# Optimization experiments

Hardware: AMD Instinct MI355X
Metric: run time of the kernel (lower is better)

Reference implementation:

```python
import jax, jax.numpy as jnp
import numpy as np

B, S, D, H, Dh = 2, 1024, 2048, 16, 128
EPS = 1e-6


def setup_inputs() -> dict:
    key = jax.random.key(0)
    ks = jax.random.split(key, 8)
    hidden_states = jax.random.normal(ks[0], (B, S, D), jnp.float32)
    def qweight(k):
        return jax.random.randint(k, (D, D), -127, 128, dtype=jnp.int32)
    wq, wk, wv, wo = qweight(ks[1]), qweight(ks[2]), qweight(ks[3]), qweight(ks[4])
    def scale(k):
        # per-output-channel dequant scale ~ O(1/(127*sqrt(D)))
        return jax.random.uniform(k, (D,), jnp.float32, 0.5, 1.5) / (127.0 * np.sqrt(D))
    wq_s, wk_s, wv_s, wo_s = scale(ks[5]), scale(ks[6]), scale(ks[7]), scale(jax.random.fold_in(key, 99))
    qn_w = jnp.ones((D,), jnp.float32)
    kn_w = jnp.ones((D,), jnp.float32)
    # RoPE tables (rotate-half convention): [S, Dh]
    pos = jnp.arange(S, dtype=jnp.float32)
    inv_freq = 1.0 / (10000.0 ** (jnp.arange(0, Dh, 2, dtype=jnp.float32) / Dh))
    freqs = pos[:, None] * inv_freq[None, :]              # [S, Dh/2]
    cos = jnp.concatenate([jnp.cos(freqs)] * 2, axis=-1)  # [S, Dh]
    sin = jnp.concatenate([jnp.sin(freqs)] * 2, axis=-1)
    lengths = jnp.array([S, 3 * S // 4], dtype=jnp.int32)
    return dict(hidden_states=hidden_states, wq_s=wq_s, wk_s=wk_s, wv_s=wv_s,
                wo_s=wo_s, qn_w=qn_w, kn_w=kn_w, cos=cos, sin=sin,
                wq=wq, wk=wk, wv=wv, wo=wo, lengths=lengths)


def _q8_linear(x, w_int, scale):
    # Q8Linear: int8 weight [out,in] dequantized by per-output-channel scale
    w = w_int.astype(jnp.float32) * scale[:, None]
    return jnp.einsum('bsd,od->bso', x, w)


def _rms_norm(x, w):
    var = jnp.mean(jnp.square(x), axis=-1, keepdims=True)
    return x * jax.lax.rsqrt(var + EPS) * w


def _apply_rope(x, cos, sin):
    # x: [B,S,D] -> per-head rotate-half RoPE -> [B,S,D]
    xh = x.reshape(B, S, H, Dh)
    x1, x2 = jnp.split(xh, 2, axis=-1)
    rot = jnp.concatenate([-x2, x1], axis=-1)
    out = xh * cos[None, :, None, :] + rot * sin[None, :, None, :]
    return out.reshape(B, S, D)


def reference(hidden_states, wq_s, wk_s, wv_s, wo_s, qn_w, kn_w, cos, sin,
              wq, wk, wv, wo, lengths):
    q = _rms_norm(_q8_linear(hidden_states, wq, wq_s), qn_w)
    k = _rms_norm(_q8_linear(hidden_states, wk, wk_s), kn_w)
    v = _q8_linear(hidden_states, wv, wv_s)
    q = _apply_rope(q, cos, sin)
    k = _apply_rope(k, cos, sin)
    # [B,S,D] -> [B,H,S,Dh]
    q = q.reshape(B, S, H, Dh).transpose(0, 2, 1, 3)
    k = k.reshape(B, S, H, Dh).transpose(0, 2, 1, 3)
    v = v.reshape(B, S, H, Dh).transpose(0, 2, 1, 3)
    # length mask -> additive bias [B,1,1,S]
    positions = jnp.arange(S)
    valid = positions[None, :] < lengths[:, None]
    bias = jnp.where(valid, 0.0, -jnp.inf).astype(jnp.float32)[:, None, None, :]
    scores = jnp.einsum('bhqd,bhkd->bhqk', q, k) / np.sqrt(Dh) + bias
    probs = jax.nn.softmax(scores, axis=-1)
    attn = jnp.einsum('bhqk,bhkd->bhqd', probs, v)
    attn = attn.transpose(0, 2, 1, 3).reshape(B, S, D)
    out = _q8_linear(attn, wo, wo_s)
    return out
```

## Files before the change

### kernel.cpp

```cpp
#include <hip/hip_runtime.h>
#include <stdint.h>

typedef __bf16 bf16;
typedef bf16 bf16x8 __attribute__((ext_vector_type(8)));
typedef bf16 bf16x4 __attribute__((ext_vector_type(4)));
typedef float f32x4 __attribute__((ext_vector_type(4)));

#define B_   2
#define S_   1024
#define D_   2048
#define H_   16
#define DH_  128
#define M_   (B_*S_)
#define EPSF 1e-6f

__device__ __forceinline__ void gload_lds16(const void* g, void* l) {
    __builtin_amdgcn_global_load_lds(
        (const __attribute__((address_space(1))) void*)g,
        (__attribute__((address_space(3))) void*)l,
        16, 0, 0);
}

struct ConvArgs {
    const void* s[5];
    bf16* d[5];
};

__global__ __launch_bounds__(256) void conv_all(ConvArgs a, int n) {
    const int z = blockIdx.y;
    const int i = (blockIdx.x * 256 + threadIdx.x) * 8;
    if (i + 8 > n) return;
    bf16x8 o;
    if (z == 0) {
        const float* src = (const float*)a.s[0];
        float4 v0 = *(const float4*)(src + i);
        float4 v1 = *(const float4*)(src + i + 4);
        o[0] = (bf16)v0.x; o[1] = (bf16)v0.y; o[2] = (bf16)v0.z; o[3] = (bf16)v0.w;
        o[4] = (bf16)v1.x; o[5] = (bf16)v1.y; o[6] = (bf16)v1.z; o[7] = (bf16)v1.w;
    } else {
        const int* src = (const int*)a.s[z];
        int4 v0 = *(const int4*)(src + i);
        int4 v1 = *(const int4*)(src + i + 4);
        o[0] = (bf16)(float)v0.x; o[1] = (bf16)(float)v0.y;
        o[2] = (bf16)(float)v0.z; o[3] = (bf16)(float)v0.w;
        o[4] = (bf16)(float)v1.x; o[5] = (bf16)(float)v1.y;
        o[6] = (bf16)(float)v1.z; o[7] = (bf16)(float)v1.w;
    }
    *(bf16x8*)(a.d[z] + i) = o;
}

struct QKVArgs {
    const float* Sc[3];
    bf16* qO; bf16* kO; bf16* vO;
};

__global__ __launch_bounds__(512, 2) void gemmQKV(const bf16* __restrict__ A, const bf16* __restrict__ Wcat,
                                                  QKVArgs args) {
    __shared__ char lds[114688];
    constexpr int NT = D_ / 64;
    constexpr int BUF = 57344;
    const int t = threadIdx.x;
    const int w = t >> 6, l = t & 63;
    const int wr = w >> 2, wc = w & 3;
    const int m0 = blockIdx.y * 256, n0 = blockIdx.x * 192;
    const int hi = l >> 4, lo = l & 15;

    const int r8 = l >> 3;
    const int ce = ((l & 7) ^ (r8 & 7)) * 8;
    const bf16* Ag = A    + (size_t)(m0 + w * 8 + r8) * D_ + ce;
    const bf16* Bg = Wcat + (size_t)(n0 + w * 8 + r8) * D_ + ce;

    auto stageA = [&](int kt, int half) {
        if (kt >= NT) return;
        const bf16* g = Ag + (size_t)(half * 128) * D_ + (size_t)kt * 64;
        char* d = lds + (kt & 1) * BUF + half * 16384 + w * 1024;
        gload_lds16((const void*)g, (void*)d);
        gload_lds16((const void*)(g + (size_t)64 * D_), (void*)(d + 8192));
    };
    auto stageB = [&](int kt) {
        if (kt >= NT) return;
        const bf16* g = Bg + (size_t)kt * 64;
        char* d = lds + (kt & 1) * BUF + 32768 + w * 1024;
        gload_lds16((const void*)g, (void*)d);
        gload_lds16((const void*)(g + (size_t)64 * D_), (void*)(d + 8192));
        gload_lds16((const void*)(g + (size_t)128 * D_), (void*)(d + 16384));
    };

    f32x4 acc[8][3] = {};

    stageA(0, 0); stageA(0, 1); stageB(0);
    stageB(1); stageA(1, 0);
    asm volatile("s_waitcnt vmcnt(5)" ::: "memory");
    asm volatile("s_barrier" ::: "memory");

    for (int kt = 0; kt < NT; ++kt) {
        const char* Pb = lds + (kt & 1) * BUF;
        const char* As = Pb;
        const char* Bs = Pb + 32768;
        bf16x8 a[4][2], b0[2], b1[2], b2[2];

        auto rdA = [&](int mi, int kk) -> bf16x8 {
            int row = wr * 128 + mi * 16 + lo;
            return *(const bf16x8*)(As + row * 128 + ((kk * 64 + hi * 16) ^ ((row & 7) << 4)));
        };
        auto rdB = [&](int ni, int kk) -> bf16x8 {
            int row = wc * 48 + ni * 16 + lo;
            return *(const bf16x8*)(Bs + row * 128 + ((kk * 64 + hi * 16) ^ ((row & 7) << 4)));
        };

#pragma unroll
        for (int mi = 0; mi < 4; ++mi) { a[mi][0] = rdA(mi, 0); a[mi][1] = rdA(mi, 1); }
        b0[0] = rdB(0, 0); b0[1] = rdB(0, 1);
        b1[0] = rdB(1, 0); b1[1] = rdB(1, 1);
        stageA(kt + 1, 1);
        asm volatile("s_barrier" ::: "memory");
        asm volatile("s_waitcnt lgkmcnt(0)" ::: "memory");
        __builtin_amdgcn_sched_barrier(0);
        __builtin_amdgcn_s_setprio(1);
#pragma unroll
        for (int mi = 0; mi < 4; ++mi)
#pragma unroll
            for (int kk = 0; kk < 2; ++kk) {
                acc[mi][0] = __builtin_amdgcn_mfma_f32_16x16x32_bf16(a[mi][kk], b0[kk], acc[mi][0], 0, 0, 0);
                acc[mi][1] = __builtin_amdgcn_mfma_f32_16x16x32_bf16(a[mi][kk], b1[kk], acc[mi][1], 0, 0, 0);
            }
        __builtin_amdgcn_s_setprio(0);
        asm volatile("s_barrier" ::: "memory");

        b2[0] = rdB(2, 0); b2[1] = rdB(2, 1);
        asm volatile("s_barrier" ::: "memory");
        asm volatile("s_waitcnt lgkmcnt(0)" ::: "memory");
        __builtin_amdgcn_sched_barrier(0);
        __builtin_amdgcn_s_setprio(1);
#pragma unroll
        for (int mi = 0; mi < 4; ++mi)
#pragma unroll
            for (int kk = 0; kk < 2; ++kk)
                acc[mi][2] = __builtin_amdgcn_mfma_f32_16x16x32_bf16(a[mi][kk], b2[kk], acc[mi][2], 0, 0, 0);
        __builtin_amdgcn_s_setprio(0);
        asm volatile("s_barrier" ::: "memory");

#pragma unroll
        for (int mi = 0; mi < 4; ++mi) { a[mi][0] = rdA(4 + mi, 0); a[mi][1] = rdA(4 + mi, 1); }
        stageB(kt + 2);
        asm volatile("s_barrier" ::: "memory");
        asm volatile("s_waitcnt lgkmcnt(0)" ::: "memory");
        __builtin_amdgcn_sched_barrier(0);
        __builtin_amdgcn_s_setprio(1);
#pragma unroll
        for (int mi = 0; mi < 4; ++mi)
#pragma unroll
            for (int kk = 0; kk < 2; ++kk) {
                acc[4 + mi][1] = __builtin_amdgcn_mfma_f32_16x16x32_bf16(a[mi][kk], b1[kk], acc[4 + mi][1], 0, 0, 0);
                acc[4 + mi][2] = __builtin_amdgcn_mfma_f32_16x16x32_bf16(a[mi][kk], b2[kk], acc[4 + mi][2], 0, 0, 0);
            }
        __builtin_amdgcn_s_setprio(0);
        asm volatile("s_barrier" ::: "memory");

        stageA(kt + 2, 0);
        asm volatile("s_barrier" ::: "memory");
        __builtin_amdgcn_sched_barrier(0);
        __builtin_amdgcn_s_setprio(1);
#pragma unroll
        for (int mi = 0; mi < 4; ++mi)
#pragma unroll
            for (int kk = 0; kk < 2; ++kk)
                acc[4 + mi][0] = __builtin_amdgcn_mfma_f32_16x16x32_bf16(a[mi][kk], b0[kk], acc[4 + mi][0], 0, 0, 0);
        __builtin_amdgcn_s_setprio(0);
        if (kt < NT - 2) asm volatile("s_waitcnt vmcnt(5)" ::: "memory");
        else             asm volatile("s_waitcnt vmcnt(0)" ::: "memory");
        asm volatile("s_barrier" ::: "memory");
    }

#pragma unroll
    for (int ni = 0; ni < 3; ++ni) {
        const int n = n0 + wc * 48 + ni * 16 + lo;
        const int z = n >> 11, col = n & 2047;
        const float scv = args.Sc[z][col];
#pragma unroll
        for (int mi = 0; mi < 8; ++mi) {
            const int mb = m0 + wr * 128 + mi * 16 + hi * 4;
            if (z == 2) {
                bf16x4 pk;
#pragma unroll
                for (int r = 0; r < 4; ++r) pk[r] = (bf16)(acc[mi][ni][r] * scv);
                const int bb = mb >> 10, s = mb & 1023, hh = col >> 7, dh = col & 127;
                *(bf16x4*)(args.vO + (((size_t)(bb * H_ + hh)) * DH_ + dh) * S_ + s) = pk;
            } else {
                bf16* dst = (z == 0 ? args.qO : args.kO);
#pragma unroll
                for (int r = 0; r < 4; ++r)
                    dst[(size_t)(mb + r) * D_ + col] = (bf16)(acc[mi][ni][r] * scv);
            }
        }
    }
}

__global__ __launch_bounds__(256, 2) void gemmO(const bf16* __restrict__ A, const bf16* __restrict__ W,
                                                const float* __restrict__ Sc, float* __restrict__ O) {
    __shared__ char lds[65536];
    constexpr int NT = D_ / 64;
    const int t = threadIdx.x;
    const int w = t >> 6, l = t & 63;
    const int wr = w >> 1, wc = w & 1;
    const int m0 = blockIdx.y * 128, n0 = blockIdx.x * 128;
    const int hi = l >> 4, lo = l & 15;

    const int r8 = l >> 3;
    const int ce = ((l & 7) ^ (r8 & 7)) * 8;
    const bf16* Ag = A + (size_t)(m0 + w * 8 + r8) * D_ + ce;
    const bf16* Bg = W + (size_t)(n0 + w * 8 + r8) * D_ + ce;

    auto stage = [&](int kt) {
        char* d = lds + (kt & 1) * 32768 + w * 1024;
        const bf16* ga = Ag + (size_t)kt * 64;
        const bf16* gb = Bg + (size_t)kt * 64;
#pragma unroll
        for (int j = 0; j < 4; ++j) {
            gload_lds16((const void*)(ga + (size_t)j * 32 * D_), (void*)(d + j * 4096));
            gload_lds16((const void*)(gb + (size_t)j * 32 * D_), (void*)(d + 16384 + j * 4096));
        }
    };

    f32x4 acc[4][4] = {};
    stage(0);
    for (int kt = 0; kt < NT; ++kt) {
        const char* cur = lds + (kt & 1) * 32768;
        if (kt + 1 < NT) {
            stage(kt + 1);
            asm volatile("s_waitcnt vmcnt(8)" ::: "memory");
        } else {
            asm volatile("s_waitcnt vmcnt(0)" ::: "memory");
        }
        asm volatile("s_barrier" ::: "memory");

        bf16x8 a[4][2], b[4][2];
#pragma unroll
        for (int mi = 0; mi < 4; ++mi)
#pragma unroll
            for (int kk = 0; kk < 2; ++kk) {
                int row = wr * 64 + mi * 16 + lo;
                a[mi][kk] = *(const bf16x8*)(cur + row * 128 + ((kk * 64 + hi * 16) ^ ((row & 7) << 4)));
            }
#pragma unroll
        for (int ni = 0; ni < 4; ++ni)
#pragma unroll
            for (int kk = 0; kk < 2; ++kk) {
                int row = wc * 64 + ni * 16 + lo;
                b[ni][kk] = *(const bf16x8*)(cur + 16384 + row * 128 + ((kk * 64 + hi * 16) ^ ((row & 7) << 4)));
            }
        __builtin_amdgcn_s_setprio(1);
#pragma unroll
        for (int mi = 0; mi < 4; ++mi)
#pragma unroll
            for (int ni = 0; ni < 4; ++ni)
#pragma unroll
                for (int kk = 0; kk < 2; ++kk)
                    acc[mi][ni] = __builtin_amdgcn_mfma_f32_16x16x32_bf16(a[mi][kk], b[ni][kk], acc[mi][ni], 0, 0, 0);
        __builtin_amdgcn_s_setprio(0);
        asm volatile("s_barrier" ::: "memory");
    }

#pragma unroll
    for (int ni = 0; ni < 4; ++ni) {
        const int n = n0 + wc * 64 + ni * 16 + lo;
        const float scv = Sc[n];
#pragma unroll
        for (int mi = 0; mi < 4; ++mi) {
            const int mb = m0 + wr * 64 + mi * 16 + hi * 4;
#pragma unroll
            for (int r = 0; r < 4; ++r)
                O[(size_t)(mb + r) * D_ + n] = acc[mi][ni][r] * scv;
        }
    }
}

__global__ __launch_bounds__(256) void rope_norm(const bf16* __restrict__ qr, const bf16* __restrict__ kr,
                                                 const float* __restrict__ qn, const float* __restrict__ kn,
                                                 const float* __restrict__ cosT, const float* __restrict__ sinT,
                                                 bf16* __restrict__ qOut, bf16* __restrict__ kOut) {
    const int which = blockIdx.z;
    const bf16* src = which ? kr : qr;
    const float* nw = which ? kn : qn;
    bf16* dst = which ? kOut : qOut;
    const int row = blockIdx.x;
    const int b = row >> 10, s = row & 1023;
    const int t = threadIdx.x;
    __shared__ float xs[D_];
    __shared__ float red[4];

    bf16x8 v = *(const bf16x8*)(src + (size_t)row * D_ + t * 8);
    float x[8]; float ss = 0.f;
#pragma unroll
    for (int j = 0; j < 8; ++j) { x[j] = (float)v[j]; ss += x[j] * x[j]; xs[t * 8 + j] = x[j]; }
#pragma unroll
    for (int msk = 32; msk; msk >>= 1) ss += __shfl_xor(ss, msk, 64);
    if ((t & 63) == 0) red[t >> 6] = ss;
    __syncthreads();
    const float inv = rsqrtf((red[0] + red[1] + red[2] + red[3]) / (float)D_ + EPSF);

    const int h = t >> 4;
    const int dh0 = (t & 15) * 8;
    bf16x8 o;
#pragma unroll
    for (int j = 0; j < 8; ++j) {
        int dd = dh0 + j;
        int d = h * 128 + dd;
        int pd = (dd < 64) ? d + 64 : d - 64;
        float xn = x[j] * inv * nw[d];
        float xp = xs[pd] * inv * nw[pd];
        float rot = (dd < 64) ? -xp : xp;
        o[j] = (bf16)(xn * cosT[s * DH_ + dd] + rot * sinT[s * DH_ + dd]);
    }
    *(bf16x8*)(dst + (((size_t)(b * H_ + h)) * S_ + s) * DH_ + dh0) = o;
}

__global__ __launch_bounds__(256) void flash(const bf16* __restrict__ Q, const bf16* __restrict__ Kb,
                                             const bf16* __restrict__ VTb, const int* __restrict__ lengths,
                                             bf16* __restrict__ Out) {
    __shared__ bf16 Qs[64 * 128];
    __shared__ bf16 Ks[64 * 128];
    __shared__ bf16 Vt[128 * 64];
    __shared__ bf16 Ps[4][16 * 64];
    const int t = threadIdx.x, w = t >> 6, l = t & 63;
    const int bh = blockIdx.y;
    const int b = bh >> 4;
    const int q0 = blockIdx.x * 64;
    const int L = lengths[b];
    const size_t base = (size_t)bh * S_ * DH_;
    const size_t vbase = (size_t)bh * DH_ * S_;
    const int hi = l >> 4, lo = l & 15;
    const int swz = (lo & 7) << 3;

    {
        const bf16* src = Q + base + (size_t)q0 * DH_;
#pragma unroll
        for (int i = 0; i < 4; ++i) {
            int r = (w * 4 + i) * 4 + (l >> 4);
            int sb = ((l & 15) * 16) ^ ((r & 7) << 4);
            gload_lds16((const void*)(src + (size_t)r * DH_ + (sb >> 1)), (void*)(Qs + (w * 4 + i) * 512));
        }
    }

    f32x4 O[8] = {};
    float mrow[4], lrow[4];
#pragma unroll
    for (int r = 0; r < 4; ++r) { mrow[r] = -1e30f; lrow[r] = 0.f; }
    const int nt = (L + 63) >> 6;
    const float sscale = 0.08838834764831843f;

    for (int kt = 0; kt < nt; ++kt) {
        const int k0 = kt * 64;
        __syncthreads();
        {
            const bf16* ksrc = Kb + base + (size_t)k0 * DH_;
#pragma unroll
            for (int i = 0; i < 4; ++i) {
                int r = (w * 4 + i) * 4 + (l >> 4);
                int sb = ((l & 15) * 16) ^ ((r & 7) << 4);
                gload_lds16((const void*)(ksrc + (size_t)r * DH_ + (sb >> 1)), (void*)(Ks + (w * 4 + i) * 512));
            }
        }
        {
            const bf16* vsrc = VTb + vbase + k0;
#pragma unroll
            for (int i = 0; i < 4; ++i) {
                int d = (w * 4 + i) * 8 + (l >> 3);
                int sb = ((l & 7) * 16) ^ ((d & 7) << 4);
                gload_lds16((const void*)(vsrc + (size_t)d * S_ + (sb >> 1)), (void*)(Vt + (w * 4 + i) * 512));
            }
        }
        __syncthreads();

        f32x4 sc[4] = {};
#pragma unroll
        for (int kk = 0; kk < 4; ++kk) {
            const int ko = kk * 32 + hi * 8;
            bf16x8 aq = *(const bf16x8*)(Qs + (w * 16 + lo) * 128 + (ko ^ swz));
#pragma unroll
            for (int ni = 0; ni < 4; ++ni) {
                bf16x8 bk = *(const bf16x8*)(Ks + (ni * 16 + lo) * 128 + (ko ^ swz));
                sc[ni] = __builtin_amdgcn_mfma_f32_16x16x32_bf16(aq, bk, sc[ni], 0, 0, 0);
            }
        }

        float p[4][4];
#pragma unroll
        for (int r = 0; r < 4; ++r) {
            float sv[4]; float vmax = -1e30f;
#pragma unroll
            for (int ni = 0; ni < 4; ++ni) {
                int kg = k0 + ni * 16 + lo;
                float vv = sc[ni][r] * sscale;
                if (kg >= L) vv = -1e30f;
                sv[ni] = vv;
                vmax = fmaxf(vmax, vv);
            }
#pragma unroll
            for (int msk = 1; msk < 16; msk <<= 1) vmax = fmaxf(vmax, __shfl_xor(vmax, msk, 64));
            float mnew = fmaxf(mrow[r], vmax);
            float corr = __expf(mrow[r] - mnew);
            float rs = 0.f;
#pragma unroll
            for (int ni = 0; ni < 4; ++ni) { float pv = __expf(sv[ni] - mnew); p[r][ni] = pv; rs += pv; }
#pragma unroll
            for (int msk = 1; msk < 16; msk <<= 1) rs += __shfl_xor(rs, msk, 64);
            lrow[r] = lrow[r] * corr + rs;
            mrow[r] = mnew;
#pragma unroll
            for (int di = 0; di < 8; ++di) O[di][r] *= corr;
        }

#pragma unroll
        for (int r = 0; r < 4; ++r) {
            int prow = hi * 4 + r;
#pragma unroll
            for (int ni = 0; ni < 4; ++ni)
                Ps[w][prow * 64 + (((ni * 16 + lo)) ^ ((prow & 7) << 3))] = (bf16)p[r][ni];
        }

#pragma unroll
        for (int kk = 0; kk < 2; ++kk) {
            const int ko = kk * 32 + hi * 8;
            bf16x8 ap = *(const bf16x8*)(&Ps[w][lo * 64 + (ko ^ swz)]);
#pragma unroll
            for (int di = 0; di < 8; ++di) {
                bf16x8 bv = *(const bf16x8*)(Vt + (di * 16 + lo) * 64 + (ko ^ swz));
                O[di] = __builtin_amdgcn_mfma_f32_16x16x32_bf16(ap, bv, O[di], 0, 0, 0);
            }
        }
    }

    const int h = bh & 15;
#pragma unroll
    for (int r = 0; r < 4; ++r) {
        float invl = 1.0f / lrow[r];
        int qrow = q0 + w * 16 + hi * 4 + r;
        bf16* orow = Out + (size_t)(b * S_ + qrow) * D_ + h * DH_;
#pragma unroll
        for (int di = 0; di < 8; ++di)
            orow[di * 16 + lo] = (bf16)(O[di][r] * invl);
    }
}

extern "C" void kernel_launch(void* const* d_in, const int* in_sizes, int n_in,
                              void* d_out, int out_size, void* d_ws, size_t ws_size,
                              hipStream_t stream) {
    const float* x    = (const float*)d_in[0];
    const float* wq_s = (const float*)d_in[1];
    const float* wk_s = (const float*)d_in[2];
    const float* wv_s = (const float*)d_in[3];
    const float* wo_s = (const float*)d_in[4];
    const float* qn   = (const float*)d_in[5];
    const float* kn   = (const float*)d_in[6];
    const float* cosT = (const float*)d_in[7];
    const float* sinT = (const float*)d_in[8];
    const int* wq = (const int*)d_in[9];
    const int* wk = (const int*)d_in[10];
    const int* wv = (const int*)d_in[11];
    const int* wo = (const int*)d_in[12];
    const int* lengths = (const int*)d_in[13];
    float* out = (float*)d_out;

    char* ws = (char*)d_ws;
    const size_t SLOT = (size_t)M_ * D_ * sizeof(bf16);
    bf16* xb   = (bf16*)(ws);
    bf16* wqb  = (bf16*)(ws + 1 * SLOT);
    bf16* wkb  = (bf16*)(ws + 2 * SLOT);
    bf16* wvb  = (bf16*)(ws + 3 * SLOT);
    bf16* wob  = (bf16*)(ws + 4 * SLOT);
    bf16* qr   = (bf16*)(ws + 5 * SLOT);
    bf16* kr   = (bf16*)(ws + 6 * SLOT);
    bf16* qb2  = (bf16*)(ws + 7 * SLOT);
    bf16* kb2  = (bf16*)(ws + 8 * SLOT);
    bf16* vb2  = (bf16*)(ws + 9 * SLOT);
    bf16* attnb = qr;

    const int NW = D_ * D_;
    ConvArgs ca;
    ca.s[0] = x;  ca.d[0] = xb;
    ca.s[1] = wq; ca.d[1] = wqb;
    ca.s[2] = wk; ca.d[2] = wkb;
    ca.s[3] = wv; ca.d[3] = wvb;
    ca.s[4] = wo; ca.d[4] = wob;
    conv_all<<<dim3(NW / 2048, 5), dim3(256), 0, stream>>>(ca, NW);

    QKVArgs qa;
    qa.Sc[0] = wq_s; qa.Sc[1] = wk_s; qa.Sc[2] = wv_s;
    qa.qO = qr; qa.kO = kr; qa.vO = vb2;
    gemmQKV<<<dim3(3 * D_ / 192, M_ / 256), dim3(512), 0, stream>>>(xb, wqb, qa);

    rope_norm<<<dim3(M_, 1, 2), dim3(256), 0, stream>>>(qr, kr, qn, kn, cosT, sinT, qb2, kb2);

    flash<<<dim3(S_ / 64, B_ * H_, 1), dim3(256), 0, stream>>>(qb2, kb2, vb2, lengths, attnb);

    gemmO<<<dim3(D_ / 128, M_ / 128), dim3(256), 0, stream>>>(attnb, wob, wo_s, out);
}
```

Measured before the change: 148.7 us.

## Shrink QKV GEMM tile to 128x192 with a simpler double-buffered pipeline

Halves the M tile of the fused QKV GEMM from 256 to 128 rows, which cuts LDS per block from 112KB to 80KB and doubles the grid. The launch-bounds occupancy hint rises from 2 to 4. The interleaved, multi-phase A/B staging with several barriers per K step is replaced by one prefetch of the next K tile, one wait and barrier, then all fragment reads and MFMAs. The aim is more resident blocks per CU and fewer barriers. In exchange, each block reuses its loaded B data across fewer rows, so global and LDS traffic per FLOP goes up, and the MFMA work no longer overlaps LDS reads as finely.

```diff
diff --git a/kernel.cpp b/kernel.cpp
--- a/kernel.cpp
+++ b/kernel.cpp
@@ -54,15 +54,15 @@
     bf16* qO; bf16* kO; bf16* vO;
 };
 
-__global__ __launch_bounds__(512, 2) void gemmQKV(const bf16* __restrict__ A, const bf16* __restrict__ Wcat,
+__global__ __launch_bounds__(512, 4) void gemmQKV(const bf16* __restrict__ A, const bf16* __restrict__ Wcat,
                                                   QKVArgs args) {
-    __shared__ char lds[114688];
+    __shared__ char lds[81920];
     constexpr int NT = D_ / 64;
-    constexpr int BUF = 57344;
+    constexpr int BUF = 40960;
     const int t = threadIdx.x;
     const int w = t >> 6, l = t & 63;
     const int wr = w >> 2, wc = w & 3;
-    const int m0 = blockIdx.y * 256, n0 = blockIdx.x * 192;
+    const int m0 = blockIdx.y * 128, n0 = blockIdx.x * 192;
     const int hi = l >> 4, lo = l & 15;
 
     const int r8 = l >> 3;
@@ -70,105 +70,55 @@
     const bf16* Ag = A    + (size_t)(m0 + w * 8 + r8) * D_ + ce;
     const bf16* Bg = Wcat + (size_t)(n0 + w * 8 + r8) * D_ + ce;
 
-    auto stageA = [&](int kt, int half) {
+    auto stage = [&](int kt) {
         if (kt >= NT) return;
-        const bf16* g = Ag + (size_t)(half * 128) * D_ + (size_t)kt * 64;
-        char* d = lds + (kt & 1) * BUF + half * 16384 + w * 1024;
-        gload_lds16((const void*)g, (void*)d);
-        gload_lds16((const void*)(g + (size_t)64 * D_), (void*)(d + 8192));
+        char* d = lds + (kt & 1) * BUF + w * 1024;
+        const bf16* ga = Ag + (size_t)kt * 64;
+        gload_lds16((const void*)ga, (void*)d);
+        gload_lds16((const void*)(ga + (size_t)64 * D_), (void*)(d + 8192));
+        const bf16* gb = Bg + (size_t)kt * 64;
+        gload_lds16((const void*)gb, (void*)(d + 16384));
+        gload_lds16((const void*)(gb + (size_t)64 * D_), (void*)(d + 24576));
+        gload_lds16((const void*)(gb + (size_t)128 * D_), (void*)(d + 32768));
     };
-    auto stageB = [&](int kt) {
-        if (kt >= NT) return;
-        const bf16* g = Bg + (size_t)kt * 64;
-        char* d = lds + (kt & 1) * BUF + 32768 + w * 1024;
-        gload_lds16((const void*)g, (void*)d);
-        gload_lds16((const void*)(g + (size_t)64 * D_), (void*)(d + 8192));
-        gload_lds16((const void*)(g + (size_t)128 * D_), (void*)(d + 16384));
-    };
-
-    f32x4 acc[8][3] = {};
-
-    stageA(0, 0); stageA(0, 1); stageB(0);
-    stageB(1); stageA(1, 0);
-    asm volatile("s_waitcnt vmcnt(5)" ::: "memory");
-    asm volatile("s_barrier" ::: "memory");
-
+
+    f32x4 acc[4][3] = {};
+
+    stage(0);
     for (int kt = 0; kt < NT; ++kt) {
-        const char* Pb = lds + (kt & 1) * BUF;
-        const char* As = Pb;
-        const char* Bs = Pb + 32768;
-        bf16x8 a[4][2], b0[2], b1[2], b2[2];
-
-        auto rdA = [&](int mi, int kk) -> bf16x8 {
-            int row = wr * 128 + mi * 16 + lo;
-            return *(const bf16x8*)(As + row * 128 + ((kk * 64 + hi * 16) ^ ((row & 7) << 4)));
-        };
-        auto rdB = [&](int ni, int kk) -> bf16x8 {
-            int row = wc * 48 + ni * 16 + lo;
-            return *(const bf16x8*)(Bs + row * 128 + ((kk * 64 + hi * 16) ^ ((row & 7) << 4)));
-        };
-
-#pragma unroll
-        for (int mi = 0; mi < 4; ++mi) { a[mi][0] = rdA(mi, 0); a[mi][1] = rdA(mi, 1); }
-        b0[0] = rdB(0, 0); b0[1] = rdB(0, 1);
-        b1[0] = rdB(1, 0); b1[1] = rdB(1, 1);
-        stageA(kt + 1, 1);
+        const char* cur = lds + (kt & 1) * BUF;
+        if (kt + 1 < NT) {
+            stage(kt + 1);
+            asm volatile("s_waitcnt vmcnt(5)" ::: "memory");
+        } else {
+            asm volatile("s_waitcnt vmcnt(0)" ::: "memory");
+        }
         asm volatile("s_barrier" ::: "memory");
-        asm volatile("s_waitcnt lgkmcnt(0)" ::: "memory");
-        __builtin_amdgcn_sched_barrier(0);
+
+        bf16x8 a[4][2], b[3][2];
+#pragma unroll
+        for (int mi = 0; mi < 4; ++mi)
+#pragma unroll
+            for (int kk = 0; kk < 2; ++kk) {
+                int row = wr * 64 + mi * 16 + lo;
+                a[mi][kk] = *(const bf16x8*)(cur + row * 128 + ((kk * 64 + hi * 16) ^ ((row & 7) << 4)));
+            }
+#pragma unroll
+        for (int ni = 0; ni < 3; ++ni)
+#pragma unroll
+            for (int kk = 0; kk < 2; ++kk) {
+                int row = wc * 48 + ni * 16 + lo;
+                b[ni][kk] = *(const bf16x8*)(cur + 16384 + row * 128 + ((kk * 64 + hi * 16) ^ ((row & 7) << 4)));
+            }
         __builtin_amdgcn_s_setprio(1);
 #pragma unroll
         for (int mi = 0; mi < 4; ++mi)
 #pragma unroll
-            for (int kk = 0; kk < 2; ++kk) {
-                acc[mi][0] = __builtin_amdgcn_mfma_f32_16x16x32_bf16(a[mi][kk], b0[kk], acc[mi][0], 0, 0, 0);
-                acc[mi][1] = __builtin_amdgcn_mfma_f32_16x16x32_bf16(a[mi][kk], b1[kk], acc[mi][1], 0, 0, 0);
-            }
+            for (int ni = 0; ni < 3; ++ni)
+#pragma unroll
+                for (int kk = 0; kk < 2; ++kk)
+                    acc[mi][ni] = __builtin_amdgcn_mfma_f32_16x16x32_bf16(a[mi][kk], b[ni][kk], acc[mi][ni], 0, 0, 0);
         __builtin_amdgcn_s_setprio(0);
-        asm volatile("s_barrier" ::: "memory");
-
-        b2[0] = rdB(2, 0); b2[1] = rdB(2, 1);
-        asm volatile("s_barrier" ::: "memory");
-        asm volatile("s_waitcnt lgkmcnt(0)" ::: "memory");
-        __builtin_amdgcn_sched_barrier(0);
-        __builtin_amdgcn_s_setprio(1);
-#pragma unroll
-        for (int mi = 0; mi < 4; ++mi)
-#pragma unroll
-            for (int kk = 0; kk < 2; ++kk)
-                acc[mi][2] = __builtin_amdgcn_mfma_f32_16x16x32_bf16(a[mi][kk], b2[kk], acc[mi][2], 0, 0, 0);
-        __builtin_amdgcn_s_setprio(0);
-        asm volatile("s_barrier" ::: "memory");
-
-#pragma unroll
-        for (int mi = 0; mi < 4; ++mi) { a[mi][0] = rdA(4 + mi, 0); a[mi][1] = rdA(4 + mi, 1); }
-        stageB(kt + 2);
-        asm volatile("s_barrier" ::: "memory");
-        asm volatile("s_waitcnt lgkmcnt(0)" ::: "memory");
-        __builtin_amdgcn_sched_barrier(0);
-        __builtin_amdgcn_s_setprio(1);
-#pragma unroll
-        for (int mi = 0; mi < 4; ++mi)
-#pragma unroll
-            for (int kk = 0; kk < 2; ++kk) {
-                acc[4 + mi][1] = __builtin_amdgcn_mfma_f32_16x16x32_bf16(a[mi][kk], b1[kk], acc[4 + mi][1], 0, 0, 0);
-                acc[4 + mi][2] = __builtin_amdgcn_mfma_f32_16x16x32_bf16(a[mi][kk], b2[kk], acc[4 + mi][2], 0, 0, 0);
-            }
-        __builtin_amdgcn_s_setprio(0);
-        asm volatile("s_barrier" ::: "memory");
-
-        stageA(kt + 2, 0);
-        asm volatile("s_barrier" ::: "memory");
-        __builtin_amdgcn_sched_barrier(0);
-        __builtin_amdgcn_s_setprio(1);
-#pragma unroll
-        for (int mi = 0; mi < 4; ++mi)
-#pragma unroll
-            for (int kk = 0; kk < 2; ++kk)
-                acc[4 + mi][0] = __builtin_amdgcn_mfma_f32_16x16x32_bf16(a[mi][kk], b0[kk], acc[4 + mi][0], 0, 0, 0);
-        __builtin_amdgcn_s_setprio(0);
-        if (kt < NT - 2) asm volatile("s_waitcnt vmcnt(5)" ::: "memory");
-        else             asm volatile("s_waitcnt vmcnt(0)" ::: "memory");
         asm volatile("s_barrier" ::: "memory");
     }
 
@@ -178,8 +128,8 @@
         const int z = n >> 11, col = n & 2047;
         const float scv = args.Sc[z][col];
 #pragma unroll
-        for (int mi = 0; mi < 8; ++mi) {
-            const int mb = m0 + wr * 128 + mi * 16 + hi * 4;
+        for (int mi = 0; mi < 4; ++mi) {
+            const int mb = m0 + wr * 64 + mi * 16 + hi * 4;
             if (z == 2) {
                 bf16x4 pk;
 #pragma unroll
@@ -488,7 +438,7 @@
     QKVArgs qa;
     qa.Sc[0] = wq_s; qa.Sc[1] = wk_s; qa.Sc[2] = wv_s;
     qa.qO = qr; qa.kO = kr; qa.vO = vb2;
-    gemmQKV<<<dim3(3 * D_ / 192, M_ / 256), dim3(512), 0, stream>>>(xb, wqb, qa);
+    gemmQKV<<<dim3(3 * D_ / 192, M_ / 128), dim3(512), 0, stream>>>(xb, wqb, qa);
 
     rope_norm<<<dim3(M_, 1, 2), dim3(256), 0, stream>>>(qr, kr, qn, kn, cosT, sinT, qb2, kb2);
 
```

Result: faster. 145.1 us (-2.4%).
